# Performance work log

Measured on AMD Instinct MI355X. Metric: run time of the kernel, lower is better.

Reference implementation:

```python
import jax, jax.numpy as jnp
import numpy as np

N, F, D, S = 40000, 20, 128, 512
DISCOUNT = 0.995      # HP.DISCOUNT_FACTOR
ECOEF = 0.1           # HP.ENTROPY_COEF
NEG = -1e30           # masked-logit fill (avoids -inf nan grads)


def setup_inputs() -> dict:
    key = jax.random.key(0)
    ks = jax.random.split(key, 16)
    features = jax.random.normal(ks[0], (N, F), dtype=jnp.float32)
    # passive-set membership at each SEL event (host-precomputed bookkeeping)
    sel_mask = jax.random.bernoulli(ks[1], 0.3, (S, N))
    sel_idx = jax.random.randint(ks[2], (S,), 0, N)
    sel_mask = sel_mask.at[jnp.arange(S), sel_idx].set(True)  # selected clause is passive
    proof = jax.random.bernoulli(ks[3], 0.02, (N,))
    good_mask = jnp.logical_and(sel_mask, proof[None, :])
    sc = 0.05
    params = {
        'W1': jax.random.normal(ks[4], (F, D), jnp.float32) * sc,
        'b1': jnp.zeros((D,), jnp.float32),
        'W2': jax.random.normal(ks[5], (D, D), jnp.float32) * sc,
        'b2': jnp.zeros((D,), jnp.float32),
        'init_key': jax.random.normal(ks[6], (D,), jnp.float32) * sc,    # initial LSTM h (the 'key')
        'init_state': jax.random.normal(ks[7], (D,), jnp.float32) * sc,  # initial LSTM c
        'Wih': jax.random.normal(ks[8], (4 * D, D), jnp.float32) * sc,
        'Whh': jax.random.normal(ks[9], (4 * D, D), jnp.float32) * sc,
        'bih': jnp.zeros((4 * D,), jnp.float32),
        'bhh': jnp.zeros((4 * D,), jnp.float32),
    }
    return {'features': features, 'sel_mask': sel_mask, 'good_mask': good_mask,
            'sel_idx': sel_idx, **params}


def reference(features, sel_mask, good_mask, sel_idx,
              W1, b1, W2, b2, init_key, init_state, Wih, Whh, bih, bhh):
    # clause_embedder: MLP over all clause feature vectors
    emb = jax.nn.relu(features @ W1 + b1) @ W2 + b2  # [N, D]

    def step(carry, inp):
        h, c, cnt = carry          # LSTM hidden (= key), cell, active-step count
        mask, good, idx = inp
        logits = emb @ h                                   # [N] matvec over all clauses
        ml = jnp.where(mask, logits, NEG)                  # restrict to passive set
        lsm = ml - jax.scipy.special.logsumexp(ml)         # masked log_softmax
        n_pass = jnp.sum(mask).astype(lsm.dtype)
        n_good = jnp.sum(good).astype(lsm.dtype)
        n_bad = n_pass - n_good
        active = jnp.logical_and(n_good > 0, n_bad > 0)
        # mean-reduced cross-entropy over proof clauses (USE_MIN_FOR_LOSS_REDUCE=False)
        ce = -jnp.sum(jnp.where(good, lsm, 0.0)) / jnp.maximum(n_good, 1.0)
        factor = DISCOUNT ** cnt
        term = jnp.where(active, factor * (n_bad / n_pass) * ce, 0.0)
        # normalized negative entropy: dot(exp(lsm), lsm) / log(len(passive))
        minus_ent = jnp.sum(jnp.where(mask, jnp.exp(lsm) * lsm, 0.0)) \
            / jnp.log(jnp.maximum(n_pass, 2.0))
        term = term + jnp.where(active, ECOEF * minus_ent, 0.0)
        # LSTM cell update with the selected clause's embedding (torch gate order i,f,g,o)
        x = emb[idx]
        gates = Wih @ x + bih + Whh @ h + bhh
        i, f, g, o = jnp.split(gates, 4)
        c2 = jax.nn.sigmoid(f) * c + jax.nn.sigmoid(i) * jnp.tanh(g)
        h2 = jax.nn.sigmoid(o) * jnp.tanh(c2)
        return (h2, c2, cnt + active.astype(cnt.dtype)), term

    carry0 = (init_key, init_state, jnp.zeros((), features.dtype))
    (_, _, steps), terms = jax.lax.scan(step, carry0, (sel_mask, good_mask, sel_idx))
    loss = jnp.sum(terms) / jnp.maximum(steps, 1.0)
    return loss.reshape(1)
```

## Files before the change

### kernel.cpp

```cpp
#include <hip/hip_runtime.h>
#include <stdint.h>

#define N_CL 40000
#define NF   20
#define DD   128
#define SS   512
#define NW   625
#define PARTN (NW * SS)
#define NEGF (-3.0e38f)
#define DISCOUNT 0.995f
#define ECOEF 0.1f

typedef __attribute__((ext_vector_type(2))) float f32x2;
typedef __attribute__((ext_vector_type(4))) float f32x4;
typedef __attribute__((ext_vector_type(16))) float f32x16;
typedef __attribute__((ext_vector_type(8))) short short8;
typedef __attribute__((ext_vector_type(4))) unsigned short us4;

__device__ __forceinline__ float rcpf(float x) { return __builtin_amdgcn_rcpf(x); }
__device__ __forceinline__ float sigm(float x) { return rcpf(1.f + __expf(-x)); }
__device__ __forceinline__ float tanh_fast(float x) { return 1.f - 2.f * rcpf(1.f + __expf(2.f * x)); }
__device__ __forceinline__ unsigned short f2bf(float f) {
    unsigned u = __float_as_uint(f);
    return (unsigned short)((u + 0x7fffu + ((u >> 16) & 1u)) >> 16);
}
__device__ __forceinline__ float bf2f(unsigned short s) {
    return __uint_as_float(((unsigned)s) << 16);
}

#define EMB_FMA(RR) { f32x4 hvv = *(const f32x4*)&hs[rg * 8 + RR][q]; \
    acc##RR += wv0 * hvv.x + wv1 * hvv.y + wv2 * hvv.z + wv3 * hvv.w; }
#define EMB_ST(RR) { f32x4 f = acc##RR + bv; us4 hi, lo; \
    hi[0] = f2bf(f.x); lo[0] = f2bf(f.x - bf2f(hi[0])); \
    hi[1] = f2bf(f.y); lo[1] = f2bf(f.y - bf2f(hi[1])); \
    hi[2] = f2bf(f.z); lo[2] = f2bf(f.z - bf2f(hi[2])); \
    hi[3] = f2bf(f.w); lo[3] = f2bf(f.w - bf2f(hi[3])); \
    int row_ = rbase + rg * 8 + RR; \
    *(us4*)&emb_hi[row_ * DD + c4 * 4] = hi; \
    *(us4*)&emb_lo[row_ * DD + c4 * 4] = lo; }

__global__ __launch_bounds__(256) void k_emb(const float* __restrict__ feat,
                                             const float* __restrict__ W1,
                                             const float* __restrict__ b1,
                                             const float* __restrict__ W2,
                                             const float* __restrict__ b2,
                                             unsigned short* __restrict__ emb_hi,
                                             unsigned short* __restrict__ emb_lo) {
    __shared__ float fs[64][NF];
    __shared__ float hs[64][132];
    int t = threadIdx.x;
    int rbase = blockIdx.x * 64;
    for (int i = t; i < 64 * NF; i += 256)
        fs[i / NF][i % NF] = feat[rbase * NF + i];
    __syncthreads();
    {
        int c = t & 127;
        float bb = b1[c];
#pragma unroll
        for (int k = 0; k < 32; ++k) {
            int r = (t >> 7) + 2 * k;
            float acc = bb;
#pragma unroll
            for (int f = 0; f < NF; ++f) acc += fs[r][f] * W1[f * DD + c];
            hs[r][c] = fmaxf(acc, 0.f);
        }
    }
    __syncthreads();
    int c4 = t & 31, rg = t >> 5;
    f32x4 acc0{0,0,0,0}, acc1{0,0,0,0}, acc2{0,0,0,0}, acc3{0,0,0,0},
          acc4{0,0,0,0}, acc5{0,0,0,0}, acc6{0,0,0,0}, acc7{0,0,0,0};
    for (int q = 0; q < DD; q += 4) {
        f32x4 wv0 = *(const f32x4*)&W2[(q + 0) * DD + c4 * 4];
        f32x4 wv1 = *(const f32x4*)&W2[(q + 1) * DD + c4 * 4];
        f32x4 wv2 = *(const f32x4*)&W2[(q + 2) * DD + c4 * 4];
        f32x4 wv3 = *(const f32x4*)&W2[(q + 3) * DD + c4 * 4];
        EMB_FMA(0) EMB_FMA(1) EMB_FMA(2) EMB_FMA(3)
        EMB_FMA(4) EMB_FMA(5) EMB_FMA(6) EMB_FMA(7)
    }
    f32x4 bv = *(const f32x4*)&b2[c4 * 4];
    EMB_ST(0) EMB_ST(1) EMB_ST(2) EMB_ST(3)
    EMB_ST(4) EMB_ST(5) EMB_ST(6) EMB_ST(7)
}

__global__ __launch_bounds__(256) void k_pgemm(const unsigned short* __restrict__ emb_hi,
                                               const unsigned short* __restrict__ emb_lo,
                                               const int* __restrict__ sel_idx,
                                               const float* __restrict__ Wih,
                                               const float* __restrict__ bih,
                                               const float* __restrict__ bhh,
                                               const float* __restrict__ Whh,
                                               float* __restrict__ W2T,
                                               float* __restrict__ P2) {
    if (blockIdx.x >= 64) {
        int tid = (blockIdx.x - 64) * 256 + threadIdx.x;
#pragma unroll
        for (int k = 0; k < 2; ++k) {
            int cid = tid * 2 + k;
            int w = cid >> 11;
            int i = (cid >> 6) & 31;
            int l = cid & 63;
            int r = i >> 3, q = i & 7;
            int row = (w >> 2) * 256 + l * 4 + r;
            int col = (w & 3) * 32 + q * 4;
            *(f32x4*)&W2T[cid * 4] = *(const f32x4*)&Whh[row * DD + col];
        }
        return;
    }
    __shared__ __align__(16) float x8[8][DD];
    int t = threadIdx.x;
    int sb = blockIdx.x * 8;
    for (int i = t; i < 8 * DD; i += 256) {
        int sl = i >> 7, k = i & 127;
        int idx = sel_idx[sb + sl] * DD + k;
        x8[sl][k] = bf2f(emb_hi[idx]) + bf2f(emb_lo[idx]);
    }
    __syncthreads();
    for (int jj = t; jj < 512; jj += 256) {
        float base = bih[jj] + bhh[jj];
        float acc[8];
#pragma unroll
        for (int s8 = 0; s8 < 8; ++s8) acc[s8] = base;
        const float4* wr = (const float4*)(Wih + jj * DD);
        for (int q = 0; q < 32; ++q) {
            float4 w4 = wr[q];
#pragma unroll
            for (int s8 = 0; s8 < 8; ++s8) {
                const float4* xs = (const float4*)&x8[s8][0];
                float4 xv = xs[q];
                acc[s8] += w4.x * xv.x + w4.y * xv.y + w4.z * xv.z + w4.w * xv.w;
            }
        }
        int pos = jj & 127, g = jj >> 7;
        for (int s8 = 0; s8 < 8; ++s8) P2[(sb + s8) * 512 + pos * 4 + g] = acc[s8];
    }
}

#define LO2(V) __builtin_shufflevector(V, V, 0, 1)
#define HI2(V) __builtin_shufflevector(V, V, 2, 3)
#define MQ(Q) { f32x4 hv = hp[Q]; \
    f32x2 hl = LO2(hv), hh2 = HI2(hv); \
    a0l += LO2(w0##Q) * hl; a0h += HI2(w0##Q) * hh2; \
    a1l += LO2(w1##Q) * hl; a1h += HI2(w1##Q) * hh2; \
    a2l += LO2(w2##Q) * hl; a2h += HI2(w2##Q) * hh2; \
    a3l += LO2(w3##Q) * hl; a3h += HI2(w3##Q) * hh2; }

#define STEP(J, PV) { \
    const f32x4* hp = (const f32x4*)&h_w[w][0]; \
    f32x2 a0l{0,0}, a0h{0,0}, a1l{0,0}, a1h{0,0}, \
          a2l{0,0}, a2h{0,0}, a3l{0,0}, a3h{0,0}; \
    MQ(0) MQ(1) MQ(2) MQ(3) MQ(4) MQ(5) MQ(6) MQ(7) \
    f32x4 ps; \
    ps.x = (a0l.x + a0l.y) + (a0h.x + a0h.y); \
    ps.y = (a1l.x + a1l.y) + (a1h.x + a1h.y); \
    ps.z = (a2l.x + a2l.y) + (a2h.x + a2h.y); \
    ps.w = (a3l.x + a3l.y) + (a3h.x + a3h.y); \
    *(f32x4*)&psum[(J) & 1][kq][gbase] = ps; \
    asm volatile("s_waitcnt lgkmcnt(0)\n\ts_barrier" ::: "memory"); \
    if ((J) == 0 && gh == 1 && g8 > 0) {                  \
        int pg_ = (g8 - 1) & 1; \
        _Pragma("unroll") \
        for (int u_ = 0; u_ < 2; ++u_) { \
            int jj_ = 2 * (w - 4) + u_, sp_ = (g8 - 1) * 8 + jj_; \
            float2 hv_ = *(const float2*)&h_hist[pg_][jj_][2 * l]; \
            unsigned short ah_ = f2bf(hv_.x), bh_ = f2bf(hv_.y); \
            unsigned short al_ = f2bf(hv_.x - bf2f(ah_)), bl_ = f2bf(hv_.y - bf2f(bh_)); \
            *(unsigned*)&Hhi[sp_ * DD + 2 * l] = (unsigned)ah_ | ((unsigned)bh_ << 16); \
            *(unsigned*)&Hlo[sp_ * DD + 2 * l] = (unsigned)al_ | ((unsigned)bl_ << 16); \
        } \
    } \
    float q00 = psum[(J) & 1][0][t_el],       q01 = psum[(J) & 1][1][t_el]; \
    float q02 = psum[(J) & 1][2][t_el],       q03 = psum[(J) & 1][3][t_el]; \
    float q10 = psum[(J) & 1][0][128 + t_el], q11 = psum[(J) & 1][1][128 + t_el]; \
    float q12 = psum[(J) & 1][2][128 + t_el], q13 = psum[(J) & 1][3][128 + t_el]; \
    float q20 = psum[(J) & 1][0][256 + t_el], q21 = psum[(J) & 1][1][256 + t_el]; \
    float q22 = psum[(J) & 1][2][256 + t_el], q23 = psum[(J) & 1][3][256 + t_el]; \
    float q30 = psum[(J) & 1][0][384 + t_el], q31 = psum[(J) & 1][1][384 + t_el]; \
    float q32 = psum[(J) & 1][2][384 + t_el], q33 = psum[(J) & 1][3][384 + t_el]; \
    float gi = ((q00 + q01) + (q02 + q03)) + (PV).x; \
    float gf = ((q10 + q11) + (q12 + q13)) + (PV).y; \
    float gg = ((q20 + q21) + (q22 + q23)) + (PV).z; \
    float go = ((q30 + q31) + (q32 + q33)) + (PV).w; \
    float ii = sigm(gi), ff = sigm(gf), tg = tanh_fast(gg), oo = sigm(go); \
    c = ff * c + ii * tg; \
    float hh = oo * tanh_fast(c); \
    if (l < 32) { \
        h_w[w][ln] = hh; \
        if (gh == 0) h_hist[(g8 + (((J) == 7) ? 1 : 0)) & 1][((J) + 1) & 7][t_el] = hh; \
    } \
}

__global__ __launch_bounds__(512, 1) void k_lstm(const float* __restrict__ W2T,
                                                 const float* __restrict__ P2,
                                                 const float* __restrict__ init_h,
                                                 const float* __restrict__ init_c,
                                                 unsigned short* __restrict__ Hhi,
                                                 unsigned short* __restrict__ Hlo,
                                                 const int* __restrict__ sel,
                                                 const int* __restrict__ good,
                                                 unsigned long long* __restrict__ selw,
                                                 unsigned long long* __restrict__ goodw) {
    if (blockIdx.x != 0) {
        int wave = ((blockIdx.x - 1) * 512 + threadIdx.x) >> 6;
        int lane = threadIdx.x & 63;
        for (int i = 0; i < 64; ++i) {
            int chunk = wave * 64 + i;
            int s = chunk / NW;
            int b = chunk - s * NW;
            int idx = s * N_CL + b * 64 + lane;
            unsigned long long bs = __ballot(sel[idx]  != 0);
            unsigned long long bg = __ballot(good[idx] != 0);
            if (lane == 0) { selw[b * SS + s] = bs; goodw[b * SS + s] = bg; }
        }
        return;
    }

    __shared__ __align__(16) float psum[2][4][512];
    __shared__ __align__(16) float h_w[8][32];
    __shared__ __align__(16) float h_hist[2][8][128];

    int t = threadIdx.x, w = t >> 6, l = t & 63;
    int kq = w & 3, gh = w >> 2, ln = l & 31;
    int gbase = gh * 256 + l * 4;
    int t_el = kq * 32 + ln;

    const f32x4* wT = (const f32x4*)W2T + (size_t)w * 2048 + l;
    f32x4 w00 = wT[ 0 * 64], w01 = wT[ 1 * 64], w02 = wT[ 2 * 64], w03 = wT[ 3 * 64],
          w04 = wT[ 4 * 64], w05 = wT[ 5 * 64], w06 = wT[ 6 * 64], w07 = wT[ 7 * 64];
    f32x4 w10 = wT[ 8 * 64], w11 = wT[ 9 * 64], w12 = wT[10 * 64], w13 = wT[11 * 64],
          w14 = wT[12 * 64], w15 = wT[13 * 64], w16 = wT[14 * 64], w17 = wT[15 * 64];
    f32x4 w20 = wT[16 * 64], w21 = wT[17 * 64], w22 = wT[18 * 64], w23 = wT[19 * 64],
          w24 = wT[20 * 64], w25 = wT[21 * 64], w26 = wT[22 * 64], w27 = wT[23 * 64];
    f32x4 w30 = wT[24 * 64], w31 = wT[25 * 64], w32 = wT[26 * 64], w33 = wT[27 * 64],
          w34 = wT[28 * 64], w35 = wT[29 * 64], w36 = wT[30 * 64], w37 = wT[31 * 64];

    float c = init_c[t_el];
    if (l < 32) {
        float h0 = init_h[t_el];
        h_w[w][ln] = h0;
        if (gh == 0) h_hist[0][0][t_el] = h0;
    }
    asm volatile("s_waitcnt lgkmcnt(0)\n\ts_barrier" ::: "memory");

    for (int g8 = 0; g8 < 64; ++g8) {
        const float* pb = P2 + g8 * 4096 + t_el * 4;
        f32x4 pv0 = *(const f32x4*)(pb + 0 * 512);
        f32x4 pv1 = *(const f32x4*)(pb + 1 * 512);
        f32x4 pv2 = *(const f32x4*)(pb + 2 * 512);
        f32x4 pv3 = *(const f32x4*)(pb + 3 * 512);
        STEP(0, pv0) STEP(1, pv1) STEP(2, pv2) STEP(3, pv3)
        f32x4 pv4 = *(const f32x4*)(pb + 4 * 512);
        f32x4 pv5 = *(const f32x4*)(pb + 5 * 512);
        f32x4 pv6 = *(const f32x4*)(pb + 6 * 512);
        f32x4 pv7 = *(const f32x4*)(pb + 7 * 512);
        STEP(4, pv4) STEP(5, pv5) STEP(6, pv6) STEP(7, pv7)
    }

    asm volatile("s_waitcnt lgkmcnt(0)\n\ts_barrier" ::: "memory");
    if (gh == 1) {
#pragma unroll
        for (int u = 0; u < 2; ++u) {
            int jj = 2 * (w - 4) + u, sp = 504 + jj;
            float2 hv = *(const float2*)&h_hist[1][jj][2 * l];
            unsigned short ah = f2bf(hv.x), bh = f2bf(hv.y);
            unsigned short al = f2bf(hv.x - bf2f(ah)), bl = f2bf(hv.y - bf2f(bh));
            *(unsigned*)&Hhi[sp * DD + 2 * l] = (unsigned)ah | ((unsigned)bh << 16);
            *(unsigned*)&Hlo[sp * DD + 2 * l] = (unsigned)al | ((unsigned)bl << 16);
        }
    }
}

__global__ __launch_bounds__(256, 1) void k_logits(
        const unsigned short* __restrict__ emb_hi,
        const unsigned short* __restrict__ emb_lo,
        const unsigned short* __restrict__ Hhi,
        const unsigned short* __restrict__ Hlo,
        const unsigned long long* __restrict__ selw,
        const unsigned long long* __restrict__ goodw,
        float* __restrict__ part) {
    int b = blockIdx.x;
    int t = threadIdx.x, wv = t >> 6, l = t & 63;
    int ln = l & 31, lh = l >> 5;
    int rb = b * 64;
    const short8* A0h = (const short8*)(emb_hi + (rb + ln) * DD + lh * 8);
    const short8* A0l = (const short8*)(emb_lo + (rb + ln) * DD + lh * 8);
    const short8* A1h = (const short8*)(emb_hi + (rb + 32 + ln) * DD + lh * 8);
    const short8* A1l = (const short8*)(emb_lo + (rb + 32 + ln) * DD + lh * 8);
    for (int sg = 0; sg < 4; ++sg) {
        int s0 = sg * 128 + wv * 32;
        const short8* Bhp = (const short8*)(Hhi + (s0 + ln) * DD + lh * 8);
        const short8* Blp = (const short8*)(Hlo + (s0 + ln) * DD + lh * 8);
        f32x16 acc0, acc1;
#pragma unroll
        for (int r = 0; r < 16; ++r) { acc0[r] = 0.f; acc1[r] = 0.f; }
#pragma unroll
        for (int kc = 0; kc < 8; ++kc) {
            short8 a0h = A0h[kc * 2], a0l = A0l[kc * 2];
            short8 a1h = A1h[kc * 2], a1l = A1l[kc * 2];
            short8 bh = Bhp[kc * 2], bl = Blp[kc * 2];
            acc0 = __builtin_amdgcn_mfma_f32_32x32x16_bf16(a0h, bh, acc0, 0, 0, 0);
            acc0 = __builtin_amdgcn_mfma_f32_32x32x16_bf16(a0l, bh, acc0, 0, 0, 0);
            acc0 = __builtin_amdgcn_mfma_f32_32x32x16_bf16(a0h, bl, acc0, 0, 0, 0);
            acc1 = __builtin_amdgcn_mfma_f32_32x32x16_bf16(a1h, bh, acc1, 0, 0, 0);
            acc1 = __builtin_amdgcn_mfma_f32_32x32x16_bf16(a1l, bh, acc1, 0, 0, 0);
            acc1 = __builtin_amdgcn_mfma_f32_32x32x16_bf16(a1h, bl, acc1, 0, 0, 0);
        }
        int s = s0 + ln;
        unsigned long long sw = selw[b * SS + s];
        unsigned long long gw = goodw[b * SS + s];
        float m = NEGF;
#pragma unroll
        for (int r = 0; r < 16; ++r) {
            int row = (r & 3) + 8 * (r >> 2) + 4 * lh;
            float v0 = acc0[r], v1 = acc1[r];
            m = fmaxf(m, ((sw >> row) & 1ull) ? v0 : NEGF);
            m = fmaxf(m, ((sw >> (row + 32)) & 1ull) ? v1 : NEGF);
        }
        m = fmaxf(m, __shfl_xor(m, 32));
        float se = 0.f, sl = 0.f, slg = 0.f;
#pragma unroll
        for (int r = 0; r < 16; ++r) {
            int row = (r & 3) + 8 * (r >> 2) + 4 * lh;
            float v0 = acc0[r], v1 = acc1[r];
            float e0 = ((sw >> row) & 1ull) ? __expf(v0 - m) : 0.f;
            float e1 = ((sw >> (row + 32)) & 1ull) ? __expf(v1 - m) : 0.f;
            se += e0 + e1;
            sl += e0 * v0 + e1 * v1;
            slg += (((gw >> row) & 1ull) ? v0 : 0.f)
                 + (((gw >> (row + 32)) & 1ull) ? v1 : 0.f);
        }
        se += __shfl_xor(se, 32);
        sl += __shfl_xor(sl, 32);
        slg += __shfl_xor(slg, 32);
        if (lh == 0) {
            int o = s * NW + b;
            part[0 * PARTN + o] = m;
            part[1 * PARTN + o] = se;
            part[2 * PARTN + o] = sl;
            part[3 * PARTN + o] = slg;
            part[4 * PARTN + o] = (float)__popcll(sw);
            part[5 * PARTN + o] = (float)__popcll(gw);
        }
    }
}

__global__ __launch_bounds__(64) void k_reduce(const float* __restrict__ part,
                                               float* __restrict__ Aout,
                                               float* __restrict__ Bout,
                                               float* __restrict__ actout) {
    int s = blockIdx.x;
    int t = threadIdx.x;
    float m = NEGF, se = 0.f, sl = 0.f, slg = 0.f, np = 0.f, ng = 0.f;
    for (int b = t; b < NW; b += 64) {
        int o = s * NW + b;
        float m2  = part[0 * PARTN + o];
        float se2 = part[1 * PARTN + o];
        float sl2 = part[2 * PARTN + o];
        slg += part[3 * PARTN + o];
        np  += part[4 * PARTN + o];
        ng  += part[5 * PARTN + o];
        float nm = fmaxf(m, m2);
        float a = __expf(m - nm), a2 = __expf(m2 - nm);
        se = se * a + se2 * a2;
        sl = sl * a + sl2 * a2;
        m = nm;
    }
    for (int off = 32; off > 0; off >>= 1) {
        float m2  = __shfl_xor(m, off);
        float se2 = __shfl_xor(se, off);
        float sl2 = __shfl_xor(sl, off);
        slg += __shfl_xor(slg, off);
        np  += __shfl_xor(np, off);
        ng  += __shfl_xor(ng, off);
        float nm = fmaxf(m, m2);
        float a = __expf(m - nm), a2 = __expf(m2 - nm);
        se = se * a + se2 * a2;
        sl = sl * a + sl2 * a2;
        m = nm;
    }
    if (t == 0) {
        float lse = m + logf(se);
        float nbad = np - ng;
        int active = (ng > 0.5f) && (nbad > 0.5f);
        float ce = (ng * lse - slg) / fmaxf(ng, 1.f);
        float A = (nbad / fmaxf(np, 1.f)) * ce;
        float minus_ent = sl / se - lse;
        float B = ECOEF * (minus_ent / logf(fmaxf(np, 2.0f)));
        Aout[s] = A; Bout[s] = B; actout[s] = active ? 1.f : 0.f;
    }
}

__global__ __launch_bounds__(64) void k_final(const float* __restrict__ A,
                                              const float* __restrict__ B,
                                              const float* __restrict__ act,
                                              float* __restrict__ out) {
    int lane = threadIdx.x;
    float loss = 0.f;
    int base = 0;
    for (int ch = 0; ch < 8; ++ch) {
        int s = ch * 64 + lane;
        bool a = act[s] > 0.5f;
        unsigned long long bal = __ballot(a);
        unsigned long long ltmask = (lane == 0) ? 0ull : (~0ull >> (64 - lane));
        int pre = __popcll(bal & ltmask);
        if (a) {
            float f = powf(DISCOUNT, (float)(base + pre));
            loss += f * A[s] + B[s];
        }
        base += __popcll(bal);
    }
    for (int off = 32; off > 0; off >>= 1) loss += __shfl_xor(loss, off);
    if (lane == 0) out[0] = loss / fmaxf((float)base, 1.f);
}

extern "C" void kernel_launch(void* const* d_in, const int* in_sizes, int n_in,
                              void* d_out, int out_size, void* d_ws, size_t ws_size,
                              hipStream_t stream) {
    (void)in_sizes; (void)n_in; (void)out_size; (void)ws_size;
    const float* feat    = (const float*)d_in[0];
    const int*   sel     = (const int*)d_in[1];
    const int*   good    = (const int*)d_in[2];
    const int*   sel_idx = (const int*)d_in[3];
    const float* W1      = (const float*)d_in[4];
    const float* b1      = (const float*)d_in[5];
    const float* W2      = (const float*)d_in[6];
    const float* b2      = (const float*)d_in[7];
    const float* init_h  = (const float*)d_in[8];
    const float* init_c  = (const float*)d_in[9];
    const float* Wih     = (const float*)d_in[10];
    const float* Whh     = (const float*)d_in[11];
    const float* bih     = (const float*)d_in[12];
    const float* bhh     = (const float*)d_in[13];
    float* out = (float*)d_out;
    char* ws = (char*)d_ws;

    float*          W2T    = (float*)(ws + 0);
    unsigned short* emb_hi = (unsigned short*)(ws + 20480000);
    unsigned short* emb_lo = (unsigned short*)(ws + 30720000);
    float*          P2     = (float*)(ws + 40960000);
    unsigned short* Hhi    = (unsigned short*)(ws + 42008576);
    unsigned short* Hlo    = (unsigned short*)(ws + 42139648);
    unsigned long long* selw  = (unsigned long long*)(ws + 42270720);
    unsigned long long* goodw = (unsigned long long*)(ws + 44830720);
    float*          part   = (float*)(ws + 47390720);
    float*          Aarr   = (float*)(ws + 55070720);
    float*          Barr   = (float*)(ws + 55072768);
    float*          actarr = (float*)(ws + 55074816);

    k_emb   <<<NW, 256, 0, stream>>>(feat, W1, b1, W2, b2, emb_hi, emb_lo);
    k_pgemm <<<96, 256, 0, stream>>>(emb_hi, emb_lo, sel_idx, Wih, bih, bhh,
                                     Whh, W2T, P2);
    k_lstm  <<<626, 512, 0, stream>>>(W2T, P2, init_h, init_c, Hhi, Hlo,
                                      sel, good, selw, goodw);
    k_logits<<<NW, 256, 0, stream>>>(emb_hi, emb_lo, Hhi, Hlo, selw, goodw, part);
    k_reduce<<<SS, 64, 0, stream>>>(part, Aarr, Barr, actarr);
    k_final <<<1, 64, 0, stream>>>(Aarr, Barr, actarr, out);
}
```

Baseline: 651.8 us.

## Overlap clause embedding MLP with serial LSTM via helper blocks

Removes the standalone embedding kernel. k_pgemm now recomputes the 512 selected-clause embeddings directly from features, so it no longer depends on the full embedding table. The full embedding MLP moves into the otherwise idle helper blocks of k_lstm, which already pack the mask bitmaps, so it runs alongside the serial LSTM recurrence on block 0. This takes one kernel launch and its serialization off the critical path. The cost is duplicated MLP work for the selected rows and shared memory moved into a union buffer.

```diff
diff --git a/kernel.cpp b/kernel.cpp
--- a/kernel.cpp
+++ b/kernel.cpp
@@ -28,62 +28,11 @@
     return __uint_as_float(((unsigned)s) << 16);
 }
 
-#define EMB_FMA(RR) { f32x4 hvv = *(const f32x4*)&hs[rg * 8 + RR][q]; \
-    acc##RR += wv0 * hvv.x + wv1 * hvv.y + wv2 * hvv.z + wv3 * hvv.w; }
-#define EMB_ST(RR) { f32x4 f = acc##RR + bv; us4 hi, lo; \
-    hi[0] = f2bf(f.x); lo[0] = f2bf(f.x - bf2f(hi[0])); \
-    hi[1] = f2bf(f.y); lo[1] = f2bf(f.y - bf2f(hi[1])); \
-    hi[2] = f2bf(f.z); lo[2] = f2bf(f.z - bf2f(hi[2])); \
-    hi[3] = f2bf(f.w); lo[3] = f2bf(f.w - bf2f(hi[3])); \
-    int row_ = rbase + rg * 8 + RR; \
-    *(us4*)&emb_hi[row_ * DD + c4 * 4] = hi; \
-    *(us4*)&emb_lo[row_ * DD + c4 * 4] = lo; }
-
-__global__ __launch_bounds__(256) void k_emb(const float* __restrict__ feat,
-                                             const float* __restrict__ W1,
-                                             const float* __restrict__ b1,
-                                             const float* __restrict__ W2,
-                                             const float* __restrict__ b2,
-                                             unsigned short* __restrict__ emb_hi,
-                                             unsigned short* __restrict__ emb_lo) {
-    __shared__ float fs[64][NF];
-    __shared__ float hs[64][132];
-    int t = threadIdx.x;
-    int rbase = blockIdx.x * 64;
-    for (int i = t; i < 64 * NF; i += 256)
-        fs[i / NF][i % NF] = feat[rbase * NF + i];
-    __syncthreads();
-    {
-        int c = t & 127;
-        float bb = b1[c];
-#pragma unroll
-        for (int k = 0; k < 32; ++k) {
-            int r = (t >> 7) + 2 * k;
-            float acc = bb;
-#pragma unroll
-            for (int f = 0; f < NF; ++f) acc += fs[r][f] * W1[f * DD + c];
-            hs[r][c] = fmaxf(acc, 0.f);
-        }
-    }
-    __syncthreads();
-    int c4 = t & 31, rg = t >> 5;
-    f32x4 acc0{0,0,0,0}, acc1{0,0,0,0}, acc2{0,0,0,0}, acc3{0,0,0,0},
-          acc4{0,0,0,0}, acc5{0,0,0,0}, acc6{0,0,0,0}, acc7{0,0,0,0};
-    for (int q = 0; q < DD; q += 4) {
-        f32x4 wv0 = *(const f32x4*)&W2[(q + 0) * DD + c4 * 4];
-        f32x4 wv1 = *(const f32x4*)&W2[(q + 1) * DD + c4 * 4];
-        f32x4 wv2 = *(const f32x4*)&W2[(q + 2) * DD + c4 * 4];
-        f32x4 wv3 = *(const f32x4*)&W2[(q + 3) * DD + c4 * 4];
-        EMB_FMA(0) EMB_FMA(1) EMB_FMA(2) EMB_FMA(3)
-        EMB_FMA(4) EMB_FMA(5) EMB_FMA(6) EMB_FMA(7)
-    }
-    f32x4 bv = *(const f32x4*)&b2[c4 * 4];
-    EMB_ST(0) EMB_ST(1) EMB_ST(2) EMB_ST(3)
-    EMB_ST(4) EMB_ST(5) EMB_ST(6) EMB_ST(7)
-}
-
-__global__ __launch_bounds__(256) void k_pgemm(const unsigned short* __restrict__ emb_hi,
-                                               const unsigned short* __restrict__ emb_lo,
+__global__ __launch_bounds__(256) void k_pgemm(const float* __restrict__ feat,
+                                               const float* __restrict__ W1,
+                                               const float* __restrict__ b1,
+                                               const float* __restrict__ W2,
+                                               const float* __restrict__ b2,
                                                const int* __restrict__ sel_idx,
                                                const float* __restrict__ Wih,
                                                const float* __restrict__ bih,
@@ -106,13 +55,45 @@
         }
         return;
     }
+    __shared__ __align__(16) float fs2[8][NF];
+    __shared__ __align__(16) float hid[8][DD];
     __shared__ __align__(16) float x8[8][DD];
     int t = threadIdx.x;
     int sb = blockIdx.x * 8;
-    for (int i = t; i < 8 * DD; i += 256) {
-        int sl = i >> 7, k = i & 127;
-        int idx = sel_idx[sb + sl] * DD + k;
-        x8[sl][k] = bf2f(emb_hi[idx]) + bf2f(emb_lo[idx]);
+    for (int i = t; i < 8 * NF; i += 256)
+        fs2[i / NF][i % NF] = feat[sel_idx[sb + i / NF] * NF + i % NF];
+    __syncthreads();
+    {
+        int col = t & 127, r0 = t >> 7;
+        float a0 = b1[col], a1 = a0, a2 = a0, a3 = a0;
+        for (int f = 0; f < NF; ++f) {
+            float wv = W1[f * DD + col];
+            a0 += fs2[r0 + 0][f] * wv;
+            a1 += fs2[r0 + 2][f] * wv;
+            a2 += fs2[r0 + 4][f] * wv;
+            a3 += fs2[r0 + 6][f] * wv;
+        }
+        hid[r0 + 0][col] = fmaxf(a0, 0.f);
+        hid[r0 + 2][col] = fmaxf(a1, 0.f);
+        hid[r0 + 4][col] = fmaxf(a2, 0.f);
+        hid[r0 + 6][col] = fmaxf(a3, 0.f);
+    }
+    __syncthreads();
+    {
+        int col = t & 127, r0 = t >> 7;
+        float a0 = 0.f, a1 = 0.f, a2 = 0.f, a3 = 0.f;
+        for (int q = 0; q < DD; ++q) {
+            float wv = W2[q * DD + col];
+            a0 += hid[r0 + 0][q] * wv;
+            a1 += hid[r0 + 2][q] * wv;
+            a2 += hid[r0 + 4][q] * wv;
+            a3 += hid[r0 + 6][q] * wv;
+        }
+        float bb = b2[col];
+        x8[r0 + 0][col] = a0 + bb;
+        x8[r0 + 2][col] = a1 + bb;
+        x8[r0 + 4][col] = a2 + bb;
+        x8[r0 + 6][col] = a3 + bb;
     }
     __syncthreads();
     for (int jj = t; jj < 512; jj += 256) {
@@ -189,6 +170,17 @@
     } \
 }
 
+#define EMB_FMA4(RR) { f32x4 hvv = *(const f32x4*)&hs[rg * 4 + RR][q]; \
+    acc##RR += wv0 * hvv.x + wv1 * hvv.y + wv2 * hvv.z + wv3 * hvv.w; }
+#define EMB_ST4(RR) { f32x4 f = acc##RR + bv; us4 hi, lo; \
+    hi[0] = f2bf(f.x); lo[0] = f2bf(f.x - bf2f(hi[0])); \
+    hi[1] = f2bf(f.y); lo[1] = f2bf(f.y - bf2f(hi[1])); \
+    hi[2] = f2bf(f.z); lo[2] = f2bf(f.z - bf2f(hi[2])); \
+    hi[3] = f2bf(f.w); lo[3] = f2bf(f.w - bf2f(hi[3])); \
+    int row_ = rbase + rg * 4 + RR; \
+    *(us4*)&emb_hi[row_ * DD + c4 * 4] = hi; \
+    *(us4*)&emb_lo[row_ * DD + c4 * 4] = lo; }
+
 __global__ __launch_bounds__(512, 1) void k_lstm(const float* __restrict__ W2T,
                                                  const float* __restrict__ P2,
                                                  const float* __restrict__ init_h,
@@ -198,10 +190,20 @@
                                                  const int* __restrict__ sel,
                                                  const int* __restrict__ good,
                                                  unsigned long long* __restrict__ selw,
-                                                 unsigned long long* __restrict__ goodw) {
+                                                 unsigned long long* __restrict__ goodw,
+                                                 const float* __restrict__ feat,
+                                                 const float* __restrict__ W1,
+                                                 const float* __restrict__ b1,
+                                                 const float* __restrict__ W2,
+                                                 const float* __restrict__ b2,
+                                                 unsigned short* __restrict__ emb_hi,
+                                                 unsigned short* __restrict__ emb_lo) {
+    __shared__ __align__(16) char smem[38912];
+
     if (blockIdx.x != 0) {
-        int wave = ((blockIdx.x - 1) * 512 + threadIdx.x) >> 6;
-        int lane = threadIdx.x & 63;
+        int t = threadIdx.x;
+        int wave = ((blockIdx.x - 1) * 512 + t) >> 6;
+        int lane = t & 63;
         for (int i = 0; i < 64; ++i) {
             int chunk = wave * 64 + i;
             int s = chunk / NW;
@@ -211,12 +213,42 @@
             unsigned long long bg = __ballot(good[idx] != 0);
             if (lane == 0) { selw[b * SS + s] = bs; goodw[b * SS + s] = bg; }
         }
+        float (*fs)[NF]  = (float (*)[NF])smem;
+        float (*hs)[132] = (float (*)[132])(smem + 5120);
+        int rbase = (blockIdx.x - 1) * 64;
+        for (int i = t; i < 64 * NF; i += 512)
+            fs[i / NF][i % NF] = feat[rbase * NF + i];
+        __syncthreads();
+        {
+            int cc = t & 127;
+            float bb = b1[cc];
+#pragma unroll
+            for (int k = 0; k < 16; ++k) {
+                int r = (t >> 7) + 4 * k;
+                float acc = bb;
+#pragma unroll
+                for (int f = 0; f < NF; ++f) acc += fs[r][f] * W1[f * DD + cc];
+                hs[r][cc] = fmaxf(acc, 0.f);
+            }
+        }
+        __syncthreads();
+        int c4 = t & 31, rg = t >> 5;
+        f32x4 acc0{0,0,0,0}, acc1{0,0,0,0}, acc2{0,0,0,0}, acc3{0,0,0,0};
+        for (int q = 0; q < DD; q += 4) {
+            f32x4 wv0 = *(const f32x4*)&W2[(q + 0) * DD + c4 * 4];
+            f32x4 wv1 = *(const f32x4*)&W2[(q + 1) * DD + c4 * 4];
+            f32x4 wv2 = *(const f32x4*)&W2[(q + 2) * DD + c4 * 4];
+            f32x4 wv3 = *(const f32x4*)&W2[(q + 3) * DD + c4 * 4];
+            EMB_FMA4(0) EMB_FMA4(1) EMB_FMA4(2) EMB_FMA4(3)
+        }
+        f32x4 bv = *(const f32x4*)&b2[c4 * 4];
+        EMB_ST4(0) EMB_ST4(1) EMB_ST4(2) EMB_ST4(3)
         return;
     }
 
-    __shared__ __align__(16) float psum[2][4][512];
-    __shared__ __align__(16) float h_w[8][32];
-    __shared__ __align__(16) float h_hist[2][8][128];
+    float (*psum)[4][512]  = (float (*)[4][512])smem;
+    float (*h_w)[32]       = (float (*)[32])(smem + 16384);
+    float (*h_hist)[8][128]= (float (*)[8][128])(smem + 17408);
 
     int t = threadIdx.x, w = t >> 6, l = t & 63;
     int kq = w & 3, gh = w >> 2, ln = l & 31;
@@ -446,11 +478,11 @@
     float*          Barr   = (float*)(ws + 55072768);
     float*          actarr = (float*)(ws + 55074816);
 
-    k_emb   <<<NW, 256, 0, stream>>>(feat, W1, b1, W2, b2, emb_hi, emb_lo);
-    k_pgemm <<<96, 256, 0, stream>>>(emb_hi, emb_lo, sel_idx, Wih, bih, bhh,
-                                     Whh, W2T, P2);
+    k_pgemm <<<96, 256, 0, stream>>>(feat, W1, b1, W2, b2, sel_idx,
+                                     Wih, bih, bhh, Whh, W2T, P2);
     k_lstm  <<<626, 512, 0, stream>>>(W2T, P2, init_h, init_c, Hhi, Hlo,
-                                      sel, good, selw, goodw);
+                                      sel, good, selw, goodw,
+                                      feat, W1, b1, W2, b2, emb_hi, emb_lo);
     k_logits<<<NW, 256, 0, stream>>>(emb_hi, emb_lo, Hhi, Hlo, selw, goodw, part);
     k_reduce<<<SS, 64, 0, stream>>>(part, Aarr, Barr, actarr);
     k_final <<<1, 64, 0, stream>>>(Aarr, Barr, actarr, out);
```

After: 600.1 us, median of 2. 7.9% less time.
